# Optimization experiments

Hardware: AMD Instinct MI355X
Metric: run time of the kernel (lower is better)

The kernel has to match this reference:

```python
import jax, jax.numpy as jnp
import numpy as np

H = 8  # number of heads


def setup_inputs() -> dict:
    key = jax.random.key(0)
    ks = jax.random.split(key, 5)
    B, L, D = 4, 2048, 512
    scale = 1.0 / np.sqrt(D)
    return {
        "query": jax.random.normal(ks[0], (B, L, D), dtype=jnp.float32),
        "keys": jax.random.normal(ks[1], (B, L, D), dtype=jnp.float32),
        "Wq": jax.random.normal(ks[2], (D, D), dtype=jnp.float32) * scale,
        "Wk": jax.random.normal(ks[3], (D, D), dtype=jnp.float32) * scale,
        "Wv": jax.random.normal(ks[4], (D, D), dtype=jnp.float32) * scale,
    }


def reference(query, keys, Wq, Wk, Wv):
    B, Lq, D = query.shape
    Lk = keys.shape[1]
    dh = D // H
    # Linear layers (torch nn.Linear: y = x @ W.T), then split heads.
    Q = (query @ Wq.T).reshape(B, Lq, H, dh)
    K = (keys @ Wk.T).reshape(B, Lk, H, dh)
    V = (keys @ Wv.T).reshape(B, Lk, H, dh)
    # NOTE: original scales by sqrt(key_dim) == sqrt(D), not sqrt(head_dim).
    inv_scale = 1.0 / jnp.sqrt(jnp.float32(D))
    scores = jnp.einsum("bqhd,bkhd->bhqk", Q, K) * inv_scale  # [B,H,Lq,Lk]
    attn = jax.nn.softmax(scores, axis=-1)
    # dropout_p = 0 (eval); no dropout applied.
    out = jnp.einsum("bhqk,bkhd->bqhd", attn, V).reshape(B, Lq, D)
    return out + query  # residual
```

## Files before the change

kernel.cpp:

```cpp
#include <hip/hip_runtime.h>

typedef unsigned short u16;
typedef unsigned int   u32;
typedef short  s16x8  __attribute__((ext_vector_type(8)));
typedef float  f32x16 __attribute__((ext_vector_type(16)));
typedef unsigned int u32x2 __attribute__((ext_vector_type(2)));

__device__ __forceinline__ u16 f2bf(float f) {
    union { u32 i; float f; } x; x.f = f;
    return (u16)((x.i + 0x8000u) >> 16);
}
__device__ __forceinline__ u32 cvt_pk_bf16(float a, float b) {
    u32 r;
    asm("v_cvt_pk_bf16_f32 %0, %1, %2" : "=v"(r) : "v"(a), "v"(b));
    return r;
}
__device__ __forceinline__ u32x2 pl32_swap2(u32 vdst, u32 vsrc) {
#if __has_builtin(__builtin_amdgcn_permlane32_swap)
    return __builtin_amdgcn_permlane32_swap(vdst, vsrc, false, false);
#else
    asm("v_permlane32_swap_b32 %0, %1" : "+v"(vdst), "+v"(vsrc));
    u32x2 r; r.x = vdst; r.y = vsrc; return r;
#endif
}

#define PD 512

__global__ __launch_bounds__(256) void proj_mfma(
    const float* __restrict__ query, const float* __restrict__ keys,
    const float* __restrict__ Wq, const float* __restrict__ Wk, const float* __restrict__ Wv,
    u16* __restrict__ Qo, u16* __restrict__ Ko, u16* __restrict__ Vt)
{
    const int z = blockIdx.z;
    const float* __restrict__ X = (z == 0) ? query : keys;
    const float* __restrict__ W = (z == 0) ? Wq : ((z == 1) ? Wk : Wv);
    const int bx = blockIdx.x;
    const int by = blockIdx.y;

    const float* __restrict__ Amat = (z < 2) ? X : W;
    const float* __restrict__ Bmat = (z < 2) ? W : X;
    const int a0 = ((z < 2) ? bx : by) * 128;
    const int b0 = ((z < 2) ? by : bx) * 128;

    __shared__ u16 As[128][40];
    __shared__ u16 Bs[128][40];

    const int tid  = threadIdx.x;
    const int wave = tid >> 6, lane = tid & 63;
    const int wm = wave >> 1, wn = wave & 1;
    const int l31 = lane & 31, lh = lane >> 5;

    const int srow = tid >> 1;
    const int sk   = (tid & 1) * 16;

    f32x16 acc[2][2];
    #pragma unroll
    for (int i = 0; i < 2; ++i)
        #pragma unroll
        for (int j = 0; j < 2; ++j)
            #pragma unroll
            for (int r = 0; r < 16; ++r) acc[i][j][r] = 0.f;

    float4 ra[4], rb[4];
    {
        const float* ap = Amat + (size_t)(a0 + srow) * PD + sk;
        const float* bp = Bmat + (size_t)(b0 + srow) * PD + sk;
        #pragma unroll
        for (int i = 0; i < 4; ++i) {
            ra[i] = *(const float4*)(ap + 4*i);
            rb[i] = *(const float4*)(bp + 4*i);
        }
    }

    for (int k0 = 0; k0 < PD; k0 += 32) {
        __syncthreads();
        {
            u32 aw[8], bw[8];
            #pragma unroll
            for (int i = 0; i < 4; ++i) {
                aw[2*i]   = cvt_pk_bf16(ra[i].x, ra[i].y);
                aw[2*i+1] = cvt_pk_bf16(ra[i].z, ra[i].w);
                bw[2*i]   = cvt_pk_bf16(rb[i].x, rb[i].y);
                bw[2*i+1] = cvt_pk_bf16(rb[i].z, rb[i].w);
            }
            *(uint4*)&As[srow][sk]     = *(uint4*)&aw[0];
            *(uint4*)&As[srow][sk + 8] = *(uint4*)&aw[4];
            *(uint4*)&Bs[srow][sk]     = *(uint4*)&bw[0];
            *(uint4*)&Bs[srow][sk + 8] = *(uint4*)&bw[4];
        }
        if (k0 + 32 < PD) {
            const float* ap = Amat + (size_t)(a0 + srow) * PD + (k0 + 32) + sk;
            const float* bp = Bmat + (size_t)(b0 + srow) * PD + (k0 + 32) + sk;
            #pragma unroll
            for (int i = 0; i < 4; ++i) {
                ra[i] = *(const float4*)(ap + 4*i);
                rb[i] = *(const float4*)(bp + 4*i);
            }
        }
        __syncthreads();

        #pragma unroll
        for (int ks = 0; ks < 2; ++ks) {
            s16x8 af[2], bfr[2];
            #pragma unroll
            for (int mf = 0; mf < 2; ++mf) {
                uint4 v = *(uint4*)&As[wm*64 + mf*32 + l31][ks*16 + lh*8];
                af[mf] = *(s16x8*)&v;
            }
            #pragma unroll
            for (int nf = 0; nf < 2; ++nf) {
                uint4 v = *(uint4*)&Bs[wn*64 + nf*32 + l31][ks*16 + lh*8];
                bfr[nf] = *(s16x8*)&v;
            }
            #pragma unroll
            for (int mf = 0; mf < 2; ++mf)
                #pragma unroll
                for (int nf = 0; nf < 2; ++nf)
                    acc[mf][nf] = __builtin_amdgcn_mfma_f32_32x32x16_bf16(
                        af[mf], bfr[nf], acc[mf][nf], 0, 0, 0);
        }
    }

    const float osc = (z == 0) ? (0.044194173824159216f * 1.4426950408889634f) : 1.0f;
    u16* __restrict__ O = (z == 0) ? Qo : Ko;
    #pragma unroll
    for (int mf = 0; mf < 2; ++mf)
        #pragma unroll
        for (int nf = 0; nf < 2; ++nf)
            #pragma unroll
            for (int r = 0; r < 16; ++r) {
                const int mi = a0 + wm*64 + mf*32 + (r & 3) + 8*(r >> 2) + 4*lh;
                const int ni = b0 + wn*64 + nf*32 + l31;
                const u16 v = f2bf(acc[mf][nf][r] * osc);
                if (z < 2) {
                    O[(size_t)mi * PD + ni] = v;
                } else {
                    const int bb_ = ni >> 11, ll = ni & 2047;
                    Vt[((size_t)(bb_ * 512 + mi)) * 2048 + ll] = v;
                }
            }
}

__global__ __launch_bounds__(512) void attn_mfma(
    const u16* __restrict__ Qp, const u16* __restrict__ Kp, const u16* __restrict__ Vt,
    const float* __restrict__ query, float* __restrict__ out)
{
    const int flat = blockIdx.x + 16 * blockIdx.y + 128 * blockIdx.z;
    const int src  = (flat & 7) * 64 + (flat >> 3);
    const int qt = src & 15;
    const int h  = (src >> 4) & 7;
    const int b  = src >> 7;
    const int q0 = qt * 128;
    const int L = 2048;

    __shared__ uint4 lds_u4[36864 / 16];
    u16* lds16 = (u16*)lds_u4;

    const int tid  = threadIdx.x;
    const int wave = tid >> 6;
    const int grp  = wave >> 2;
    const int sw   = wave & 3;
    const int lane = tid & 63;
    const int l31 = lane & 31, lh = lane >> 5;

    u16* gb16 = lds16 + grp * 9216;
    u16* Ks   = gb16;
    u16* Vts  = gb16 + 4608;

    const int qrow = b * L + q0 + sw * 32 + l31;
    s16x8 qf[4];
    #pragma unroll
    for (int ds = 0; ds < 4; ++ds) {
        uint4 v = *(const uint4*)(Qp + (size_t)qrow * PD + h*64 + ds*16 + lh*8);
        qf[ds] = *(s16x8*)&v;
    }

    f32x16 ot[2];
    #pragma unroll
    for (int mf = 0; mf < 2; ++mf)
        #pragma unroll
        for (int r = 0; r < 16; ++r) ot[mf][r] = 0.f;
    float l_i = 0.f;

    const int gtid = tid & 255;
    const int srow = gtid >> 2;
    const int sc   = (gtid & 3) * 16;

    const u16* kpB = Kp + (size_t)(b*L + grp*64 + srow) * PD + h*64 + sc;
    const u16* vpB = Vt + ((size_t)((b*8 + h)*64 + srow)) * 2048 + grp*64 + sc;

    uint4 rk0, rk1, rv0, rv1;

#define A_LOADG(k0v) { \
    const u16* kp_ = kpB + (size_t)(k0v) * PD; \
    const u16* vp_ = vpB + (k0v); \
    rk0 = *(const uint4*)kp_;      rk1 = *(const uint4*)(kp_ + 8); \
    rv0 = *(const uint4*)vp_;      rv1 = *(const uint4*)(vp_ + 8); }

#define A_STOREL() { \
    *(uint4*)&Ks [srow*72 + sc]      = rk0; \
    *(uint4*)&Ks [srow*72 + sc + 8]  = rk1; \
    *(uint4*)&Vts[srow*72 + sc]      = rv0; \
    *(uint4*)&Vts[srow*72 + sc + 8]  = rv1; }

    auto compute = [&]() {
        f32x16 s[2];
        #pragma unroll
        for (int kf = 0; kf < 2; ++kf) {
            #pragma unroll
            for (int r = 0; r < 16; ++r) s[kf][r] = 0.f;
            #pragma unroll
            for (int ds = 0; ds < 4; ++ds) {
                uint4 av = *(uint4*)&Ks[(kf*32 + l31)*72 + ds*16 + lh*8];
                s[kf] = __builtin_amdgcn_mfma_f32_32x32x16_bf16(
                    *(s16x8*)&av, qf[ds], s[kf], 0, 0, 0);
            }
        }
        float rs = 0.f;
        u32 pq[2][4][2];
        #pragma unroll
        for (int kf = 0; kf < 2; ++kf)
            #pragma unroll
            for (int g = 0; g < 4; ++g) {
                float p0 = __builtin_amdgcn_exp2f(s[kf][4*g+0]);
                float p1 = __builtin_amdgcn_exp2f(s[kf][4*g+1]);
                float p2 = __builtin_amdgcn_exp2f(s[kf][4*g+2]);
                float p3 = __builtin_amdgcn_exp2f(s[kf][4*g+3]);
                rs += (p0 + p1) + (p2 + p3);
                pq[kf][g][0] = cvt_pk_bf16(p0, p1);
                pq[kf][g][1] = cvt_pk_bf16(p2, p3);
            }
        rs += __shfl_xor(rs, 32);
        l_i += rs;
        #pragma unroll
        for (int s4 = 0; s4 < 4; ++s4) {
            const int kf = s4 >> 1, ga = (s4 & 1) * 2;
            u32x2 r0 = pl32_swap2(pq[kf][ga][0], pq[kf][ga+1][0]);
            u32x2 r1 = pl32_swap2(pq[kf][ga][1], pq[kf][ga+1][1]);
            union { u32 w[4]; s16x8 v; } bu;
            bu.w[0] = r0.x; bu.w[1] = r1.x; bu.w[2] = r0.y; bu.w[3] = r1.y;
            #pragma unroll
            for (int mf = 0; mf < 2; ++mf) {
                uint4 av = *(uint4*)&Vts[(mf*32 + l31)*72 + s4*16 + lh*8];
                ot[mf] = __builtin_amdgcn_mfma_f32_32x32x16_bf16(
                    *(s16x8*)&av, bu.v, ot[mf], 0, 0, 0);
            }
        }
    };

    A_LOADG(0);
    #pragma unroll 1
    for (int j = 0; j < 16; ++j) {
        __syncthreads();
        A_STOREL();
        if (j + 1 < 16) A_LOADG((j + 1) * 128);
        __syncthreads();
        __builtin_amdgcn_s_setprio(1);
        compute();
        __builtin_amdgcn_s_setprio(0);
    }

    float* Ppart = (float*)lds_u4;
    float* l_p   = Ppart + 128*68;
    float* Oe    = (float*)lds_u4;

    __syncthreads();
    if (grp == 1) {
        #pragma unroll
        for (int mf = 0; mf < 2; ++mf)
            #pragma unroll
            for (int g = 0; g < 4; ++g) {
                float4 v;
                v.x = ot[mf][g*4+0]; v.y = ot[mf][g*4+1];
                v.z = ot[mf][g*4+2]; v.w = ot[mf][g*4+3];
                const int dh0 = mf*32 + 8*g + 4*lh;
                *(float4*)&Ppart[(sw*32 + l31)*68 + dh0] = v;
            }
        if (lh == 0) l_p[sw*32 + l31] = l_i;
    }
    __syncthreads();
    if (grp == 0) {
        const float inv_l = 1.0f / (l_i + l_p[sw*32 + l31]);
        #pragma unroll
        for (int mf = 0; mf < 2; ++mf)
            #pragma unroll
            for (int g = 0; g < 4; ++g) {
                const int dh0 = mf*32 + 8*g + 4*lh;
                float4 pv = *(float4*)&Ppart[(sw*32 + l31)*68 + dh0];
                ot[mf][g*4+0] = (ot[mf][g*4+0] + pv.x) * inv_l;
                ot[mf][g*4+1] = (ot[mf][g*4+1] + pv.y) * inv_l;
                ot[mf][g*4+2] = (ot[mf][g*4+2] + pv.z) * inv_l;
                ot[mf][g*4+3] = (ot[mf][g*4+3] + pv.w) * inv_l;
            }
    }
    __syncthreads();
    if (grp == 0) {
        #pragma unroll
        for (int mf = 0; mf < 2; ++mf)
            #pragma unroll
            for (int g = 0; g < 4; ++g) {
                float4 v;
                v.x = ot[mf][g*4+0]; v.y = ot[mf][g*4+1];
                v.z = ot[mf][g*4+2]; v.w = ot[mf][g*4+3];
                const int dh0 = mf*32 + 8*g + 4*lh;
                *(float4*)&Oe[(sw*32 + l31)*68 + dh0] = v;
            }
    }
    __syncthreads();
    {
        const int r  = tid >> 2;
        const int c0 = (tid & 3) * 16;
        const size_t gb = ((size_t)(b*L + q0 + r)) * PD + h*64 + c0;
        #pragma unroll
        for (int i = 0; i < 4; ++i) {
            float4 ov = *(float4*)&Oe[r*68 + c0 + 4*i];
            float4 qv = *(const float4*)(query + gb + 4*i);
            ov.x += qv.x; ov.y += qv.y; ov.z += qv.z; ov.w += qv.w;
            *(float4*)(out + gb + 4*i) = ov;
        }
    }
}

extern "C" void kernel_launch(void* const* d_in, const int* in_sizes, int n_in,
                              void* d_out, int out_size, void* d_ws, size_t ws_size,
                              hipStream_t stream) {
    const float* query = (const float*)d_in[0];
    const float* keys  = (const float*)d_in[1];
    const float* Wq    = (const float*)d_in[2];
    const float* Wk    = (const float*)d_in[3];
    const float* Wv    = (const float*)d_in[4];
    float* out = (float*)d_out;

    u16* Qp = (u16*)d_ws;
    u16* Kp = Qp + (size_t)8192 * 512;
    u16* Vt = Kp + (size_t)8192 * 512;

    proj_mfma<<<dim3(64, 4, 3), 256, 0, stream>>>(query, keys, Wq, Wk, Wv, Qp, Kp, Vt);
    attn_mfma<<<dim3(16, 8, 4), 512, 0, stream>>>(Qp, Kp, Vt, query, out);
}
```

Before: 160.2 us.

## Load K and V MFMA fragments directly from global memory, dropping LDS staging

The attention main loop no longer stages K and V tiles through shared memory behind two barriers per iteration. Each wave now loads its MFMA operand fragments for K and V straight from global memory into registers, with the loop unrolled by two so loads can overlap compute. This removes the LDS round trip and block-wide synchronisation. In exchange, the four waves sharing a group each fetch the same K/V data redundantly from global memory or cache, and more registers are needed.

```diff
diff --git a/kernel.cpp b/kernel.cpp
--- a/kernel.cpp
+++ b/kernel.cpp
@@ -154,7 +154,6 @@
     const int L = 2048;
 
     __shared__ uint4 lds_u4[36864 / 16];
-    u16* lds16 = (u16*)lds_u4;
 
     const int tid  = threadIdx.x;
     const int wave = tid >> 6;
@@ -163,10 +162,6 @@
     const int lane = tid & 63;
     const int l31 = lane & 31, lh = lane >> 5;
 
-    u16* gb16 = lds16 + grp * 9216;
-    u16* Ks   = gb16;
-    u16* Vts  = gb16 + 4608;
-
     const int qrow = b * L + q0 + sw * 32 + l31;
     s16x8 qf[4];
     #pragma unroll
@@ -182,40 +177,39 @@
         for (int r = 0; r < 16; ++r) ot[mf][r] = 0.f;
     float l_i = 0.f;
 
-    const int gtid = tid & 255;
-    const int srow = gtid >> 2;
-    const int sc   = (gtid & 3) * 16;
-
-    const u16* kpB = Kp + (size_t)(b*L + grp*64 + srow) * PD + h*64 + sc;
-    const u16* vpB = Vt + ((size_t)((b*8 + h)*64 + srow)) * 2048 + grp*64 + sc;
-
-    uint4 rk0, rk1, rv0, rv1;
-
-#define A_LOADG(k0v) { \
-    const u16* kp_ = kpB + (size_t)(k0v) * PD; \
-    const u16* vp_ = vpB + (k0v); \
-    rk0 = *(const uint4*)kp_;      rk1 = *(const uint4*)(kp_ + 8); \
-    rv0 = *(const uint4*)vp_;      rv1 = *(const uint4*)(vp_ + 8); }
-
-#define A_STOREL() { \
-    *(uint4*)&Ks [srow*72 + sc]      = rk0; \
-    *(uint4*)&Ks [srow*72 + sc + 8]  = rk1; \
-    *(uint4*)&Vts[srow*72 + sc]      = rv0; \
-    *(uint4*)&Vts[srow*72 + sc + 8]  = rv1; }
-
-    auto compute = [&]() {
+    const u16* kbase = Kp + ((size_t)(b*L + grp*64 + l31)) * PD + h*64 + lh*8;
+    const u16* vbase = Vt + ((size_t)((b*8 + h)*64 + l31)) * 2048 + grp*64 + lh*8;
+
+    #pragma unroll 2
+    for (int j = 0; j < 16; ++j) {
+        const int kb = j * 128;
+
+        uint4 kfr[2][4];
+        #pragma unroll
+        for (int kf = 0; kf < 2; ++kf)
+            #pragma unroll
+            for (int ds = 0; ds < 4; ++ds)
+                kfr[kf][ds] = *(const uint4*)(kbase + (size_t)(kb + kf*32) * PD + ds*16);
+
+        __builtin_amdgcn_s_setprio(1);
         f32x16 s[2];
         #pragma unroll
         for (int kf = 0; kf < 2; ++kf) {
             #pragma unroll
             for (int r = 0; r < 16; ++r) s[kf][r] = 0.f;
             #pragma unroll
-            for (int ds = 0; ds < 4; ++ds) {
-                uint4 av = *(uint4*)&Ks[(kf*32 + l31)*72 + ds*16 + lh*8];
+            for (int ds = 0; ds < 4; ++ds)
                 s[kf] = __builtin_amdgcn_mfma_f32_32x32x16_bf16(
-                    *(s16x8*)&av, qf[ds], s[kf], 0, 0, 0);
-            }
-        }
+                    *(s16x8*)&kfr[kf][ds], qf[ds], s[kf], 0, 0, 0);
+        }
+
+        uint4 vfr[2][4];
+        #pragma unroll
+        for (int mf = 0; mf < 2; ++mf)
+            #pragma unroll
+            for (int s4 = 0; s4 < 4; ++s4)
+                vfr[mf][s4] = *(const uint4*)(vbase + (size_t)(mf*32) * 2048 + kb + s4*16);
+
         float rs = 0.f;
         u32 pq[2][4][2];
         #pragma unroll
@@ -232,6 +226,7 @@
             }
         rs += __shfl_xor(rs, 32);
         l_i += rs;
+
         #pragma unroll
         for (int s4 = 0; s4 < 4; ++s4) {
             const int kf = s4 >> 1, ga = (s4 & 1) * 2;
@@ -240,23 +235,10 @@
             union { u32 w[4]; s16x8 v; } bu;
             bu.w[0] = r0.x; bu.w[1] = r1.x; bu.w[2] = r0.y; bu.w[3] = r1.y;
             #pragma unroll
-            for (int mf = 0; mf < 2; ++mf) {
-                uint4 av = *(uint4*)&Vts[(mf*32 + l31)*72 + s4*16 + lh*8];
+            for (int mf = 0; mf < 2; ++mf)
                 ot[mf] = __builtin_amdgcn_mfma_f32_32x32x16_bf16(
-                    *(s16x8*)&av, bu.v, ot[mf], 0, 0, 0);
-            }
-        }
-    };
-
-    A_LOADG(0);
-    #pragma unroll 1
-    for (int j = 0; j < 16; ++j) {
-        __syncthreads();
-        A_STOREL();
-        if (j + 1 < 16) A_LOADG((j + 1) * 128);
-        __syncthreads();
-        __builtin_amdgcn_s_setprio(1);
-        compute();
+                    *(s16x8*)&vfr[mf][s4], bu.v, ot[mf], 0, 0, 0);
+        }
         __builtin_amdgcn_s_setprio(0);
     }
 
```

New measurement: 236.4 us. 1.48x slower.
